# Optimization experiments

Hardware: AMD Instinct MI355X
Metric: run time of the kernel (lower is better)

The kernel has to match this reference:

```python
import jax, jax.numpy as jnp
import numpy as np

# Module constants (from init_kwargs)
M = 5          # frames per burst; query taken from frame M//2
WS = 8         # window_size
OW = 12        # overlap_wsize = int(WS*0.5) + WS
PAD = 2        # (OW - WS) // 2
NHEADS = 8
E = 64         # embed_dim
HD = E // NHEADS  # head_dim = 8


def setup_inputs() -> dict:
    key = jax.random.key(0)
    ks = jax.random.split(key, 9)
    B, H, W = 1, 128, 128
    return {
        "x": jax.random.normal(ks[0], (B * M, 3, H, W), jnp.float32),
        "w_high": jax.random.normal(ks[1], (E, 3), jnp.float32) * 0.1,
        "b_high": jnp.zeros((E,), jnp.float32),
        "gamma": jnp.ones((E,), jnp.float32),
        "beta": jnp.zeros((E,), jnp.float32),
        "w_qkv": jax.random.normal(ks[2], (3 * E, E), jnp.float32) * 0.05,
        "pos_q": jax.random.normal(ks[3], (WS * WS, E), jnp.float32) * 0.02,
        "pos_k": jax.random.normal(ks[4], (OW * OW, E), jnp.float32) * 0.02,
        "w_out": jax.random.normal(ks[5], (E, E), jnp.float32) * 0.05,
        "w_rgb": jax.random.normal(ks[6], (3, E), jnp.float32) * 0.1,
        "b_rgb": jnp.zeros((3,), jnp.float32),
    }


def _layernorm(x, g, b, eps=1e-6):
    mu = jnp.mean(x, axis=-1, keepdims=True)
    var = jnp.mean((x - mu) ** 2, axis=-1, keepdims=True)
    return (x - mu) * jax.lax.rsqrt(var + eps) * g + b


def _unfold_windows(t):
    # t: [BM, E, H, W] -> overlapping OWxOW windows, stride WS, pad PAD
    # returns [BM*n*n, OW*OW, E]  (matches torch Unfold + 'b (c j) i -> (b i) j c')
    BM, C, H, W = t.shape
    tp = jnp.pad(t, ((0, 0), (0, 0), (PAD, PAD), (PAD, PAD)))
    n = (H + 2 * PAD - OW) // WS + 1
    rows = jnp.arange(n)[:, None] * WS + jnp.arange(OW)[None, :]  # [n, OW]
    p = tp[:, :, rows, :]          # [BM, C, n, OW, Wp]
    p = p[:, :, :, :, rows]        # [BM, C, n, OW, n, OW]
    p = p.transpose(0, 2, 4, 3, 5, 1)  # [BM, n, n, OW, OW, C]
    return p.reshape(BM * n * n, OW * OW, C)


def reference(x, w_high, b_high, gamma, beta, w_qkv, pos_q, pos_k, w_out, w_rgb, b_rgb):
    BM, _, H, W = x.shape
    B = BM // M
    # 1x1 conv 3 -> E
    feat = jnp.einsum('bchw,ec->behw', x, w_high) + b_high[None, :, None, None]
    # layernorm over channels (as sequence [BM, HW, E])
    xs = feat.reshape(BM, E, H * W).transpose(0, 2, 1)
    xs = _layernorm(xs, gamma, beta)
    # qkv projection (no bias)
    qkv = (xs @ w_qkv.T).reshape(BM, H, W, 3, E)
    Q = qkv[..., 0, :].transpose(0, 3, 1, 2)  # [BM, E, H, W]
    K = qkv[..., 1, :].transpose(0, 3, 1, 2)
    V = qkv[..., 2, :].transpose(0, 3, 1, 2)
    # broadcast the middle-frame query across all M frames
    Qb = Q.reshape(B, M, E, H, W)
    Q = jnp.broadcast_to(Qb[:, M // 2:M // 2 + 1], (B, M, E, H, W)).reshape(BM, E, H, W)
    nH, nW = H // WS, W // WS
    # non-overlapping query windows
    Qw = Q.reshape(BM, E, nH, WS, nW, WS).transpose(0, 2, 4, 3, 5, 1).reshape(-1, WS * WS, E)
    # overlapping key/value halo windows
    Kw = _unfold_windows(K)
    Vw = _unfold_windows(V)
    Qw = Qw + pos_q
    Kw = Kw + pos_k
    s = Qw.shape[0]
    q = Qw.reshape(s, WS * WS, NHEADS, HD)
    k = Kw.reshape(s, OW * OW, NHEADS, HD)
    v = Vw.reshape(s, OW * OW, NHEADS, HD)
    # attention with flash-attn default scale head_dim**-0.5
    att = jnp.einsum('sqhd,skhd->shqk', q, k) * (HD ** -0.5)
    att = jax.nn.softmax(att, axis=-1)
    out = jnp.einsum('shqk,skhd->sqhd', att, v)  # [s, WS*WS, NHEADS, HD]
    # '(b nh nw) (ph pw) h d -> b (nh ph nw pw) (h d)'
    out = out.reshape(BM, nH, nW, WS, WS, E).transpose(0, 1, 3, 2, 4, 5).reshape(BM, H * W, E)
    out = out @ w_out.T
    mixed = out.reshape(BM, H, W, E).transpose(0, 3, 1, 2) + feat
    rgb = jnp.einsum('behw,ce->bchw', mixed, w_rgb) + b_rgb[None, :, None, None]
    return rgb.reshape(B, -1, H, W)
```

## Files before the change

kernel.cpp:

```cpp
#include <hip/hip_runtime.h>
#include <hip/hip_bf16.h>

#define HW 16384
#define W_IMG 128
#define BM_TOT 5
#define PRE 0.5101179482f

typedef __attribute__((ext_vector_type(8))) short bf16x8;
typedef __attribute__((ext_vector_type(4))) float f32x4;

__device__ __forceinline__ short f2b(float f) {
    __hip_bfloat16 h = __float2bfloat16(f);
    union { __hip_bfloat16 h; short s; } c; c.h = h; return c.s;
}
__device__ __forceinline__ float b2f(short s) {
    union { unsigned u; float f; } v; v.u = ((unsigned)(unsigned short)s) << 16;
    return v.f;
}
__device__ __forceinline__ unsigned pk2(float a, float b) {
    __hip_bfloat162 h = __float22bfloat162_rn(make_float2(a, b));
    union { __hip_bfloat162 h; unsigned u; } c; c.h = h; return c.u;
}
__device__ __forceinline__ float fexp2(float x) {
#if __has_builtin(__builtin_amdgcn_exp2f)
    return __builtin_amdgcn_exp2f(x);
#else
    float r; asm("v_exp_f32 %0, %1" : "=v"(r) : "v"(x)); return r;
#endif
}

__global__ __launch_bounds__(256) void k_qkv(
    const float* __restrict__ x, const float* __restrict__ w_qkv,
    const float* __restrict__ w_high, const float* __restrict__ b_high,
    const float* __restrict__ gamma, const float* __restrict__ beta,
    const float* __restrict__ pos_q, const float* __restrict__ w_rgb,
    const float* __restrict__ w_out,
    float* __restrict__ featrgb, short* __restrict__ qmid,
    short* __restrict__ kbuf, short* __restrict__ vbuf,
    short* __restrict__ wcombb)
{
    __shared__ char smem[39680];
    short* XS  = (short*)smem;
    short* TLk = (short*)(smem + 9216);
    short* TLv = (short*)(smem + 18432);
    short* TLq = (short*)(smem + 27648);
    float* WL  = (float*)(smem + 36864);
    float* WRL = (float*)(smem + 36864 + 2048);

    const int tid = threadIdx.x, blk = blockIdx.x;
    const int bm = blk >> 8, p0 = (blk & 255) * 64;
    const int pixbase = blk * 64;
    const int wv = tid >> 6, lane = tid & 63;
    const int col = lane & 15, grp = lane >> 4;

    const int px_l = tid >> 2, part = tid & 3;
    const int p_glob = p0 + px_l;
    const float* xp = x + (size_t)bm * 3 * HW + p_glob;
    const float x0 = xp[0], x1 = xp[HW], x2 = xp[2 * HW];

    if (tid < 64) {
        WL[tid * 8 + 0] = w_high[tid * 3];
        WL[tid * 8 + 1] = w_high[tid * 3 + 1];
        WL[tid * 8 + 2] = w_high[tid * 3 + 2];
        WL[tid * 8 + 3] = b_high[tid];
        WL[tid * 8 + 4] = gamma[tid];
        WL[tid * 8 + 5] = beta[tid];
    } else if (tid < 112) {
        ((float4*)WRL)[tid - 64] = ((const float4*)w_rgb)[tid - 64];
    }
    __syncthreads();

    {
        float f[16]; float s = 0.f, s2 = 0.f;
        #pragma unroll
        for (int j = 0; j < 16; ++j) {
            const int ch = part * 16 + j;
            float4 wa = *(const float4*)&WL[ch * 8];
            f[j] = fmaf(wa.x, x0, fmaf(wa.y, x1, fmaf(wa.z, x2, wa.w)));
            s += f[j]; s2 = fmaf(f[j], f[j], s2);
        }
        float r0 = 0.f, r1 = 0.f, r2 = 0.f;
        #pragma unroll
        for (int j = 0; j < 16; ++j) {
            const float fj = f[j];
            r0 = fmaf(fj, WRL[part * 16 + j], r0);
            r1 = fmaf(fj, WRL[64 + part * 16 + j], r1);
            r2 = fmaf(fj, WRL[128 + part * 16 + j], r2);
        }
        s  += __shfl_xor(s, 1);  s  += __shfl_xor(s, 2);
        s2 += __shfl_xor(s2, 1); s2 += __shfl_xor(s2, 2);
        r0 += __shfl_xor(r0, 1); r0 += __shfl_xor(r0, 2);
        r1 += __shfl_xor(r1, 1); r1 += __shfl_xor(r1, 2);
        r2 += __shfl_xor(r2, 1); r2 += __shfl_xor(r2, 2);
        if (part < 3) {
            float rv = part == 0 ? r0 : (part == 1 ? r1 : r2);
            featrgb[((size_t)bm * 3 + part) * HW + p_glob] = rv;
        }
        const float mu = s * 0.015625f;
        const float var = s2 * 0.015625f - mu * mu;
        const float rs = rsqrtf(var + 1e-6f);
        unsigned xw[8];
        #pragma unroll
        for (int j2 = 0; j2 < 8; ++j2) {
            const int ch = part * 16 + 2 * j2;
            float4 g0 = *(const float4*)&WL[ch * 8 + 4];
            float4 g1 = *(const float4*)&WL[ch * 8 + 12];
            xw[j2] = pk2((f[2 * j2] - mu) * rs * g0.x + g0.y,
                         (f[2 * j2 + 1] - mu) * rs * g1.x + g1.y);
        }
        *(uint4*)&XS[px_l * 72 + part * 16]     = make_uint4(xw[0], xw[1], xw[2], xw[3]);
        *(uint4*)&XS[px_l * 72 + part * 16 + 8] = make_uint4(xw[4], xw[5], xw[6], xw[7]);
    }

    bf16x8 Bf[3][2];
    #pragma unroll
    for (int jj = 0; jj < 3; ++jj) {
        int jt = wv + jj * 4;
        #pragma unroll
        for (int kc = 0; kc < 2; ++kc) {
            const float4* src = (const float4*)&w_qkv[(jt * 16 + col) * 64 + kc * 32 + grp * 8];
            float4 a = src[0], b = src[1];
            union { bf16x8 v; unsigned u[4]; } tmp;
            tmp.u[0] = pk2(a.x, a.y); tmp.u[1] = pk2(a.z, a.w);
            tmp.u[2] = pk2(b.x, b.y); tmp.u[3] = pk2(b.z, b.w);
            Bf[jj][kc] = tmp.v;
        }
    }
    __syncthreads();

    #pragma unroll
    for (int pt = 0; pt < 4; ++pt) {
        bf16x8 A0 = *(const bf16x8*)&XS[(pt * 16 + col) * 72 + grp * 8];
        bf16x8 A1 = *(const bf16x8*)&XS[(pt * 16 + col) * 72 + 32 + grp * 8];

        f32x4 aK = {0.f, 0.f, 0.f, 0.f};
        aK = __builtin_amdgcn_mfma_f32_16x16x32_bf16(Bf[1][0], A0, aK, 0, 0, 0);
        aK = __builtin_amdgcn_mfma_f32_16x16x32_bf16(Bf[1][1], A1, aK, 0, 0, 0);
        uint2 kw = {pk2(aK[0], aK[1]), pk2(aK[2], aK[3])};
        *(uint2*)&TLk[(pt * 16 + col) * 72 + wv * 16 + grp * 4] = kw;

        f32x4 aV = {0.f, 0.f, 0.f, 0.f};
        aV = __builtin_amdgcn_mfma_f32_16x16x32_bf16(A0, Bf[2][0], aV, 0, 0, 0);
        aV = __builtin_amdgcn_mfma_f32_16x16x32_bf16(A1, Bf[2][1], aV, 0, 0, 0);
        #pragma unroll
        for (int i = 0; i < 4; ++i)
            TLv[(pt * 16 + grp * 4 + i) * 72 + wv * 16 + col] = f2b(aV[i]);

        if (bm == 2) {
            f32x4 aQ = {0.f, 0.f, 0.f, 0.f};
            aQ = __builtin_amdgcn_mfma_f32_16x16x32_bf16(Bf[0][0], A0, aQ, 0, 0, 0);
            aQ = __builtin_amdgcn_mfma_f32_16x16x32_bf16(Bf[0][1], A1, aQ, 0, 0, 0);
            int p = p0 + pt * 16 + col;
            int qq = ((p >> 7) & 7) * 8 + (p & 7);
            float4 pq = *(const float4*)&pos_q[qq * 64 + wv * 16 + grp * 4];
            uint2 qw = {pk2((aQ[0] + pq.x) * PRE, (aQ[1] + pq.y) * PRE),
                        pk2((aQ[2] + pq.z) * PRE, (aQ[3] + pq.w) * PRE)};
            *(uint2*)&TLq[(pt * 16 + col) * 72 + wv * 16 + grp * 4] = qw;
        }
    }
    __syncthreads();

    #pragma unroll
    for (int it = 0; it < 2; ++it) {
        int j = it * 256 + tid;
        int row = j >> 3, seg = j & 7;
        *(uint4*)&kbuf[((size_t)pixbase + row) * 64 + seg * 8] =
            *(const uint4*)&TLk[row * 72 + seg * 8];
        *(uint4*)&vbuf[((size_t)pixbase + row) * 64 + seg * 8] =
            *(const uint4*)&TLv[row * 72 + seg * 8];
        if (bm == 2)
            *(uint4*)&qmid[((size_t)p0 + row) * 64 + seg * 8] =
                *(const uint4*)&TLq[row * 72 + seg * 8];
    }

    if (blk == 0) {
        float* WOL = (float*)TLk;
        __syncthreads();
        for (int i = tid; i < 4096; i += 256) WOL[i] = w_out[i];
        __syncthreads();
        for (int i = tid; i < 1024; i += 256) {
            short wc = 0;
            if (i < 192) {
                int c = i >> 6, e = i & 63;
                float a = 0.f;
                #pragma unroll 8
                for (int e2 = 0; e2 < 64; ++e2)
                    a = fmaf(WRL[c * 64 + e2], WOL[e2 * 64 + e], a);
                wc = f2b(a);
            }
            wcombb[i] = wc;
        }
    }
}

__global__ __launch_bounds__(512, 6) void k_attn(
    const short* __restrict__ qmid, const short* __restrict__ kbuf,
    const short* __restrict__ vbuf,
    const float* __restrict__ pos_k, const float* __restrict__ b_rgb,
    const float* __restrict__ featrgb, const short* __restrict__ wcombb,
    float* __restrict__ outp)
{
    __shared__ char smem[48448];
    short* Klds = (short*)smem;
    short* Vt   = (short*)(smem + 20736);
    short* OL   = (short*)smem;

    const int tid = threadIdx.x, blk = blockIdx.x;
    const int bm = blk >> 8, widx = blk & 255;
    const int wi = widx >> 4, wj = widx & 15;
    const int head = tid >> 6, lane = tid & 63;
    const int col = lane & 15, grp = lane >> 4;

    uint4 qraw[4] = {{0,0,0,0},{0,0,0,0},{0,0,0,0},{0,0,0,0}};
    if (grp == 0) {
        #pragma unroll
        for (int qt = 0; qt < 4; ++qt) {
            int q = qt * 16 + col;
            int pix = (wi * 8 + (q >> 3)) * W_IMG + wj * 8 + (q & 7);
            qraw[qt] = *(const uint4*)&qmid[(size_t)pix * 64 + head * 8];
        }
    }

    #pragma unroll
    for (int i = 0; i < 3; ++i) {
        const int kk = lane + i * 64;
        if (i == 2 && lane >= 16) continue;
        const int r = kk / 12, c = kk - r * 12;
        const int hh = wi * 8 - 2 + r, ww = wj * 8 - 2 + c;
        uint4 kraw = {0, 0, 0, 0}, vraw = {0, 0, 0, 0};
        if ((unsigned)hh < 128u && (unsigned)ww < 128u) {
            size_t off = ((size_t)bm * HW + hh * W_IMG + ww) * 64 + head * 8;
            kraw = *(const uint4*)&kbuf[off];
            vraw = *(const uint4*)&vbuf[off];
        }
        const float* pk = &pos_k[kk * 64 + head * 8];
        float4 pk0 = *(const float4*)pk;
        float4 pk1 = *(const float4*)(pk + 4);
        union { uint4 q; short s[8]; } ku, vu;
        ku.q = kraw; vu.q = vraw;
        uint4 ko;
        ko.x = pk2(b2f(ku.s[0]) + pk0.x, b2f(ku.s[1]) + pk0.y);
        ko.y = pk2(b2f(ku.s[2]) + pk0.z, b2f(ku.s[3]) + pk0.w);
        ko.z = pk2(b2f(ku.s[4]) + pk1.x, b2f(ku.s[5]) + pk1.y);
        ko.w = pk2(b2f(ku.s[6]) + pk1.z, b2f(ku.s[7]) + pk1.w);
        *(uint4*)&Klds[kk * 72 + head * 8] = ko;
        #pragma unroll
        for (int cc = 0; cc < 8; ++cc)
            Vt[(head * 8 + cc) * 152 + kk] = vu.s[cc];
    }
    if (lane < 8) *(uint4*)&Vt[(head * 8 + lane) * 152 + 144] = (uint4){0, 0, 0, 0};
    if (head == 7 && lane == 0) *(uint4*)&Vt[64 * 152] = (uint4){0, 0, 0, 0};

    unsigned* PBh = (unsigned*)(smem + 40224 + head * 1024);
    const int slot_w = (grp * 16 + (col ^ grp)) * 4;
    const int g0 = 2 * (grp & 1);
    const int slotr1 = (g0 * 16 + (col ^ g0)) * 4 + (grp >> 1) * 2;
    const int slotr2 = ((g0 + 1) * 16 + (col ^ (g0 + 1))) * 4 + (grp >> 1) * 2;

    f32x4 oacc[4];
    float linv[4];

    #pragma unroll
    for (int qt = 0; qt < 4; ++qt) {
        union { bf16x8 v; uint4 r; } qu; qu.r = qraw[qt];
        const bf16x8 qf = qu.v;

        float l = 0.f;
        unsigned pw[20];
        __builtin_amdgcn_s_setprio(1);
        #pragma unroll
        for (int t = 0; t < 9; ++t) {
            bf16x8 kf = *(const bf16x8*)&Klds[(t * 16 + col) * 72 + head * 8];
            f32x4 sct = __builtin_amdgcn_mfma_f32_16x16x32_bf16(
                kf, qf, (f32x4){0.f, 0.f, 0.f, 0.f}, 0, 0, 0);
            float e0 = fexp2(sct[0]), e1 = fexp2(sct[1]);
            float e2 = fexp2(sct[2]), e3 = fexp2(sct[3]);
            l += (e0 + e1) + (e2 + e3);
            pw[2 * t]     = pk2(e0, e1);
            pw[2 * t + 1] = pk2(e2, e3);
        }
        __builtin_amdgcn_s_setprio(0);
        pw[18] = 0u; pw[19] = 0u;
        l += __shfl_xor(l, 16);
        l += __shfl_xor(l, 32);
        linv[qt] = __builtin_amdgcn_rcpf(l);

        *(uint4*)(PBh + slot_w) = make_uint4(pw[0], pw[1], pw[2], pw[3]);
        f32x4 oa = {0.f, 0.f, 0.f, 0.f};
        __builtin_amdgcn_s_setprio(1);
        #pragma unroll
        for (int kt2 = 0; kt2 < 5; ++kt2) {
            uint2 r1 = *(const uint2*)(PBh + slotr1);
            uint2 r2 = *(const uint2*)(PBh + slotr2);
            if (kt2 < 4)
                *(uint4*)(PBh + slot_w) =
                    make_uint4(pw[4 * kt2 + 4], pw[4 * kt2 + 5], pw[4 * kt2 + 6], pw[4 * kt2 + 7]);
            union { bf16x8 v; unsigned u[4]; } pf;
            pf.u[0] = r1.x; pf.u[1] = r1.y; pf.u[2] = r2.x; pf.u[3] = r2.y;
            bf16x8 vf = *(const bf16x8*)&Vt[(head * 8 + (lane & 7)) * 152 + kt2 * 32 + grp * 8];
            oa = __builtin_amdgcn_mfma_f32_16x16x32_bf16(vf, pf.v, oa, 0, 0, 0);
        }
        __builtin_amdgcn_s_setprio(0);
        oacc[qt] = oa;
    }

    if (grp < 2) {
        #pragma unroll
        for (int qt = 0; qt < 4; ++qt) {
            float s = linv[qt];
            uint2 ow;
            ow.x = pk2(oacc[qt][0] * s, oacc[qt][1] * s);
            ow.y = pk2(oacc[qt][2] * s, oacc[qt][3] * s);
            *(uint2*)&OL[(qt * 16 + col) * 72 + head * 8 + grp * 4] = ow;
        }
    }
    __syncthreads();

    if (head < 4) {
        const int qt = head;
        f32x4 acc = {0.f, 0.f, 0.f, 0.f};
        #pragma unroll
        for (int kc = 0; kc < 2; ++kc) {
            bf16x8 ao = *(const bf16x8*)&OL[(qt * 16 + col) * 72 + kc * 32 + grp * 8];
            bf16x8 bo = *(const bf16x8*)&wcombb[col * 64 + kc * 32 + grp * 8];
            acc = __builtin_amdgcn_mfma_f32_16x16x32_bf16(ao, bo, acc, 0, 0, 0);
        }
        if (col < 3) {
            float br = b_rgb[col];
            const float* frp = featrgb + ((size_t)bm * 3 + col) * HW;
            #pragma unroll
            for (int i = 0; i < 4; ++i) {
                int qs = qt * 16 + grp * 4 + i;
                int pix = (wi * 8 + (qs >> 3)) * W_IMG + wj * 8 + (qs & 7);
                outp[(size_t)bm * 3 * HW + col * HW + pix] = acc[i] + frp[pix] + br;
            }
        }
    }
}

extern "C" void kernel_launch(void* const* d_in, const int* in_sizes, int n_in,
                              void* d_out, int out_size, void* d_ws, size_t ws_size,
                              hipStream_t stream) {
    const float* x      = (const float*)d_in[0];
    const float* w_high = (const float*)d_in[1];
    const float* b_high = (const float*)d_in[2];
    const float* gamma  = (const float*)d_in[3];
    const float* beta   = (const float*)d_in[4];
    const float* w_qkv  = (const float*)d_in[5];
    const float* pos_q  = (const float*)d_in[6];
    const float* pos_k  = (const float*)d_in[7];
    const float* w_out  = (const float*)d_in[8];
    const float* w_rgb  = (const float*)d_in[9];
    const float* b_rgb  = (const float*)d_in[10];
    float* out = (float*)d_out;

    float* featrgb = (float*)d_ws;
    short* kbuf    = (short*)(featrgb + (size_t)BM_TOT * 3 * HW);
    short* vbuf    = kbuf + (size_t)BM_TOT * HW * 64;
    short* qmid    = vbuf + (size_t)BM_TOT * HW * 64;
    short* wcombb  = qmid + (size_t)HW * 64;

    k_qkv<<<BM_TOT * 256, 256, 0, stream>>>(x, w_qkv, w_high, b_high, gamma, beta,
                                            pos_q, w_rgb, w_out,
                                            featrgb, qmid, kbuf, vbuf, wcombb);
    k_attn<<<BM_TOT * 256, 512, 0, stream>>>(qmid, kbuf, vbuf, pos_k,
                                             b_rgb, featrgb, wcombb, out);
}
```

Before: 54.85 us.

## Split query tiles across two wave groups and keep K in registers via shuffles

The attention kernel now launches 1024 threads per window, so each head is handled by two waves that each own half of the query tiles. K tiles are no longer staged in LDS; they stay in registers and are shared through cross-lane shuffles. The QK, exp and PV steps are interleaved inside one loop instead of two phases with a 20-word register buffer. This aims to raise parallelism and cut LDS traffic, but every K/V halo tile is now loaded twice (once per wave group), many shuffles are added, and the larger blocks may reduce how many blocks fit per CU.

```diff
diff --git a/kernel.cpp b/kernel.cpp
--- a/kernel.cpp
+++ b/kernel.cpp
@@ -193,131 +193,145 @@
     }
 }
 
-__global__ __launch_bounds__(512, 6) void k_attn(
+__global__ __launch_bounds__(1024, 8) void k_attn(
     const short* __restrict__ qmid, const short* __restrict__ kbuf,
     const short* __restrict__ vbuf,
     const float* __restrict__ pos_k, const float* __restrict__ b_rgb,
     const float* __restrict__ featrgb, const short* __restrict__ wcombb,
     float* __restrict__ outp)
 {
-    __shared__ char smem[48448];
-    short* Klds = (short*)smem;
-    short* Vt   = (short*)(smem + 20736);
-    short* OL   = (short*)smem;
+    __shared__ char smem[45120];
+    short* Vt = (short*)smem;
+    short* OL = (short*)(smem + 35904);
 
     const int tid = threadIdx.x, blk = blockIdx.x;
     const int bm = blk >> 8, widx = blk & 255;
     const int wi = widx >> 4, wj = widx & 15;
-    const int head = tid >> 6, lane = tid & 63;
+    const int w = tid >> 6, lane = tid & 63;
+    const int head = w & 7, qh = w >> 3;
     const int col = lane & 15, grp = lane >> 4;
 
-    uint4 qraw[4] = {{0,0,0,0},{0,0,0,0},{0,0,0,0},{0,0,0,0}};
+    uint4 qraw[2] = {{0, 0, 0, 0}, {0, 0, 0, 0}};
     if (grp == 0) {
         #pragma unroll
-        for (int qt = 0; qt < 4; ++qt) {
-            int q = qt * 16 + col;
+        for (int qt = 0; qt < 2; ++qt) {
+            int q = (qh * 2 + qt) * 16 + col;
             int pix = (wi * 8 + (q >> 3)) * W_IMG + wj * 8 + (q & 7);
             qraw[qt] = *(const uint4*)&qmid[(size_t)pix * 64 + head * 8];
         }
     }
 
+    uint4 stgK0 = {0,0,0,0}, stgK1 = {0,0,0,0}, stgK2 = {0,0,0,0};
     #pragma unroll
     for (int i = 0; i < 3; ++i) {
         const int kk = lane + i * 64;
-        if (i == 2 && lane >= 16) continue;
-        const int r = kk / 12, c = kk - r * 12;
-        const int hh = wi * 8 - 2 + r, ww = wj * 8 - 2 + c;
-        uint4 kraw = {0, 0, 0, 0}, vraw = {0, 0, 0, 0};
-        if ((unsigned)hh < 128u && (unsigned)ww < 128u) {
-            size_t off = ((size_t)bm * HW + hh * W_IMG + ww) * 64 + head * 8;
-            kraw = *(const uint4*)&kbuf[off];
-            vraw = *(const uint4*)&vbuf[off];
-        }
-        const float* pk = &pos_k[kk * 64 + head * 8];
-        float4 pk0 = *(const float4*)pk;
-        float4 pk1 = *(const float4*)(pk + 4);
-        union { uint4 q; short s[8]; } ku, vu;
-        ku.q = kraw; vu.q = vraw;
-        uint4 ko;
-        ko.x = pk2(b2f(ku.s[0]) + pk0.x, b2f(ku.s[1]) + pk0.y);
-        ko.y = pk2(b2f(ku.s[2]) + pk0.z, b2f(ku.s[3]) + pk0.w);
-        ko.z = pk2(b2f(ku.s[4]) + pk1.x, b2f(ku.s[5]) + pk1.y);
-        ko.w = pk2(b2f(ku.s[6]) + pk1.z, b2f(ku.s[7]) + pk1.w);
-        *(uint4*)&Klds[kk * 72 + head * 8] = ko;
-        #pragma unroll
-        for (int cc = 0; cc < 8; ++cc)
-            Vt[(head * 8 + cc) * 152 + kk] = vu.s[cc];
+        const bool active = (i < 2) || (lane < 16);
+        uint4 ko = {0, 0, 0, 0};
+        if (active) {
+            const int r = kk / 12, c = kk - r * 12;
+            const int hh = wi * 8 - 2 + r, ww = wj * 8 - 2 + c;
+            uint4 kraw = {0, 0, 0, 0}, vraw = {0, 0, 0, 0};
+            if ((unsigned)hh < 128u && (unsigned)ww < 128u) {
+                size_t off = ((size_t)bm * HW + hh * W_IMG + ww) * 64 + head * 8;
+                kraw = *(const uint4*)&kbuf[off];
+                vraw = *(const uint4*)&vbuf[off];
+            }
+            const float* pk = &pos_k[kk * 64 + head * 8];
+            float4 pk0 = *(const float4*)pk;
+            float4 pk1 = *(const float4*)(pk + 4);
+            union { uint4 q; short s[8]; } ku, vu;
+            ku.q = kraw; vu.q = vraw;
+            ko.x = pk2(b2f(ku.s[0]) + pk0.x, b2f(ku.s[1]) + pk0.y);
+            ko.y = pk2(b2f(ku.s[2]) + pk0.z, b2f(ku.s[3]) + pk0.w);
+            ko.z = pk2(b2f(ku.s[4]) + pk1.x, b2f(ku.s[5]) + pk1.y);
+            ko.w = pk2(b2f(ku.s[6]) + pk1.z, b2f(ku.s[7]) + pk1.w);
+            #pragma unroll
+            for (int cc = 0; cc < 8; ++cc)
+                Vt[(head * 8 + cc) * 152 + kk] = vu.s[cc];
+        }
+        if (i == 0) stgK0 = ko; else if (i == 1) stgK1 = ko; else stgK2 = ko;
     }
     if (lane < 8) *(uint4*)&Vt[(head * 8 + lane) * 152 + 144] = (uint4){0, 0, 0, 0};
     if (head == 7 && lane == 0) *(uint4*)&Vt[64 * 152] = (uint4){0, 0, 0, 0};
 
-    unsigned* PBh = (unsigned*)(smem + 40224 + head * 1024);
+    unsigned* PBh = (unsigned*)(smem + 19520 + w * 1024);
     const int slot_w = (grp * 16 + (col ^ grp)) * 4;
     const int g0 = 2 * (grp & 1);
     const int slotr1 = (g0 * 16 + (col ^ g0)) * 4 + (grp >> 1) * 2;
     const int slotr2 = ((g0 + 1) * 16 + (col ^ (g0 + 1))) * 4 + (grp >> 1) * 2;
-
-    f32x4 oacc[4];
-    float linv[4];
-
-    #pragma unroll
-    for (int qt = 0; qt < 4; ++qt) {
+    const int vtbase = (head * 8 + (lane & 7)) * 152 + grp * 8;
+
+    f32x4 oacc[2];
+    float linv[2];
+
+    #pragma unroll
+    for (int qt = 0; qt < 2; ++qt) {
         union { bf16x8 v; uint4 r; } qu; qu.r = qraw[qt];
         const bf16x8 qf = qu.v;
 
         float l = 0.f;
-        unsigned pw[20];
+        f32x4 oa = {0.f, 0.f, 0.f, 0.f};
         __builtin_amdgcn_s_setprio(1);
         #pragma unroll
-        for (int t = 0; t < 9; ++t) {
-            bf16x8 kf = *(const bf16x8*)&Klds[(t * 16 + col) * 72 + head * 8];
-            f32x4 sct = __builtin_amdgcn_mfma_f32_16x16x32_bf16(
-                kf, qf, (f32x4){0.f, 0.f, 0.f, 0.f}, 0, 0, 0);
-            float e0 = fexp2(sct[0]), e1 = fexp2(sct[1]);
-            float e2 = fexp2(sct[2]), e3 = fexp2(sct[3]);
-            l += (e0 + e1) + (e2 + e3);
-            pw[2 * t]     = pk2(e0, e1);
-            pw[2 * t + 1] = pk2(e2, e3);
+        for (int kt2 = 0; kt2 < 5; ++kt2) {
+            unsigned w0, w1, w2 = 0u, w3 = 0u;
+            {
+                const int ta = 2 * kt2;
+                const int src = ((ta & 3) << 4) + col;
+                const uint4 sg = (ta >> 2) == 0 ? stgK0 : ((ta >> 2) == 1 ? stgK1 : stgK2);
+                union { bf16x8 v; unsigned u[4]; } kf;
+                kf.u[0] = __shfl(sg.x, src); kf.u[1] = __shfl(sg.y, src);
+                kf.u[2] = __shfl(sg.z, src); kf.u[3] = __shfl(sg.w, src);
+                f32x4 sct = __builtin_amdgcn_mfma_f32_16x16x32_bf16(
+                    kf.v, qf, (f32x4){0.f, 0.f, 0.f, 0.f}, 0, 0, 0);
+                float e0 = fexp2(sct[0]), e1 = fexp2(sct[1]);
+                float e2 = fexp2(sct[2]), e3 = fexp2(sct[3]);
+                l += (e0 + e1) + (e2 + e3);
+                w0 = pk2(e0, e1); w1 = pk2(e2, e3);
+            }
+            if (kt2 < 4) {
+                const int tb = 2 * kt2 + 1;
+                const int src = ((tb & 3) << 4) + col;
+                const uint4 sg = (tb >> 2) == 0 ? stgK0 : stgK1;
+                union { bf16x8 v; unsigned u[4]; } kf;
+                kf.u[0] = __shfl(sg.x, src); kf.u[1] = __shfl(sg.y, src);
+                kf.u[2] = __shfl(sg.z, src); kf.u[3] = __shfl(sg.w, src);
+                f32x4 sct = __builtin_amdgcn_mfma_f32_16x16x32_bf16(
+                    kf.v, qf, (f32x4){0.f, 0.f, 0.f, 0.f}, 0, 0, 0);
+                float e0 = fexp2(sct[0]), e1 = fexp2(sct[1]);
+                float e2 = fexp2(sct[2]), e3 = fexp2(sct[3]);
+                l += (e0 + e1) + (e2 + e3);
+                w2 = pk2(e0, e1); w3 = pk2(e2, e3);
+            }
+            *(uint4*)(PBh + slot_w) = make_uint4(w0, w1, w2, w3);
+            uint2 r1 = *(const uint2*)(PBh + slotr1);
+            uint2 r2 = *(const uint2*)(PBh + slotr2);
+            union { bf16x8 v; unsigned u[4]; } pf;
+            pf.u[0] = r1.x; pf.u[1] = r1.y; pf.u[2] = r2.x; pf.u[3] = r2.y;
+            bf16x8 vf = *(const bf16x8*)&Vt[vtbase + kt2 * 32];
+            oa = __builtin_amdgcn_mfma_f32_16x16x32_bf16(vf, pf.v, oa, 0, 0, 0);
         }
         __builtin_amdgcn_s_setprio(0);
-        pw[18] = 0u; pw[19] = 0u;
         l += __shfl_xor(l, 16);
         l += __shfl_xor(l, 32);
         linv[qt] = __builtin_amdgcn_rcpf(l);
-
-        *(uint4*)(PBh + slot_w) = make_uint4(pw[0], pw[1], pw[2], pw[3]);
-        f32x4 oa = {0.f, 0.f, 0.f, 0.f};
-        __builtin_amdgcn_s_setprio(1);
-        #pragma unroll
-        for (int kt2 = 0; kt2 < 5; ++kt2) {
-            uint2 r1 = *(const uint2*)(PBh + slotr1);
-            uint2 r2 = *(const uint2*)(PBh + slotr2);
-            if (kt2 < 4)
-                *(uint4*)(PBh + slot_w) =
-                    make_uint4(pw[4 * kt2 + 4], pw[4 * kt2 + 5], pw[4 * kt2 + 6], pw[4 * kt2 + 7]);
-            union { bf16x8 v; unsigned u[4]; } pf;
-            pf.u[0] = r1.x; pf.u[1] = r1.y; pf.u[2] = r2.x; pf.u[3] = r2.y;
-            bf16x8 vf = *(const bf16x8*)&Vt[(head * 8 + (lane & 7)) * 152 + kt2 * 32 + grp * 8];
-            oa = __builtin_amdgcn_mfma_f32_16x16x32_bf16(vf, pf.v, oa, 0, 0, 0);
-        }
-        __builtin_amdgcn_s_setprio(0);
         oacc[qt] = oa;
     }
 
     if (grp < 2) {
         #pragma unroll
-        for (int qt = 0; qt < 4; ++qt) {
+        for (int qt = 0; qt < 2; ++qt) {
             float s = linv[qt];
             uint2 ow;
             ow.x = pk2(oacc[qt][0] * s, oacc[qt][1] * s);
             ow.y = pk2(oacc[qt][2] * s, oacc[qt][3] * s);
-            *(uint2*)&OL[(qt * 16 + col) * 72 + head * 8 + grp * 4] = ow;
+            *(uint2*)&OL[((qh * 2 + qt) * 16 + col) * 72 + head * 8 + grp * 4] = ow;
         }
     }
     __syncthreads();
 
-    if (head < 4) {
-        const int qt = head;
+    if (w < 4) {
+        const int qt = w;
         f32x4 acc = {0.f, 0.f, 0.f, 0.f};
         #pragma unroll
         for (int kc = 0; kc < 2; ++kc) {
@@ -363,6 +377,6 @@
     k_qkv<<<BM_TOT * 256, 256, 0, stream>>>(x, w_qkv, w_high, b_high, gamma, beta,
                                             pos_q, w_rgb, w_out,
                                             featrgb, qmid, kbuf, vbuf, wcombb);
-    k_attn<<<BM_TOT * 256, 512, 0, stream>>>(qmid, kbuf, vbuf, pos_k,
-                                             b_rgb, featrgb, wcombb, out);
-}
+    k_attn<<<BM_TOT * 256, 1024, 0, stream>>>(qmid, kbuf, vbuf, pos_k,
+                                              b_rgb, featrgb, wcombb, out);
+}
```

Result: slower. 149.4 us (+172.4%).
